# Kernel optimization log

Hardware: AMD Instinct MI355X
Metric: run time of the kernel (lower is better)

Reference implementation:

```python
import jax, jax.numpy as jnp
import numpy as np

B, C, H, W = 8, 16, 512, 512


def setup_inputs() -> dict:
    key = jax.random.key(0)
    k1, k2 = jax.random.split(key)
    src = jax.random.normal(k1, (B, C, H, W), dtype=jnp.float32)
    flow = jax.random.normal(k2, (B, 2, H, W), dtype=jnp.float32)
    return {"src": src, "flow": flow}


def _warp(src, flow):
    b, c, h, w = src.shape
    # identity grid: channel 0 = row index (y), channel 1 = col index (x)
    gy, gx = jnp.meshgrid(jnp.arange(h, dtype=jnp.float32),
                          jnp.arange(w, dtype=jnp.float32), indexing='ij')
    new_y = gy[None, :, :] + flow[:, 0]   # [B,H,W]
    new_x = gx[None, :, :] + flow[:, 1]   # [B,H,W]
    # normalize to [-1,1] (as the torch module does) ...
    ny = 2.0 * (new_y / (h - 1) - 0.5)
    nx = 2.0 * (new_x / (w - 1) - 0.5)
    # ... then un-normalize as grid_sample(align_corners=True) does
    py = (ny + 1.0) * 0.5 * (h - 1)
    px = (nx + 1.0) * 0.5 * (w - 1)
    # padding_mode='border': clip source coords before computing weights
    py = jnp.clip(py, 0.0, h - 1)
    px = jnp.clip(px, 0.0, w - 1)
    y0f = jnp.floor(py)
    x0f = jnp.floor(px)
    wy = (py - y0f)[:, None, :, :]   # [B,1,H,W]
    wx = (px - x0f)[:, None, :, :]
    y0 = jnp.clip(y0f.astype(jnp.int32), 0, h - 1)
    x0 = jnp.clip(x0f.astype(jnp.int32), 0, w - 1)
    y1 = jnp.clip(y0 + 1, 0, h - 1)
    x1 = jnp.clip(x0 + 1, 0, w - 1)

    def gather(s, yi, xi):
        return s[:, yi, xi]  # [C,H,W]

    g = jax.vmap(gather)
    v00 = g(src, y0, x0)
    v01 = g(src, y0, x1)
    v10 = g(src, y1, x0)
    v11 = g(src, y1, x1)
    return (v00 * (1.0 - wy) * (1.0 - wx)
            + v01 * (1.0 - wy) * wx
            + v10 * wy * (1.0 - wx)
            + v11 * wy * wx)


def reference(src, flow):
    return _warp(src, flow)
```

## Files before the change

### kernel.cpp

```cpp
#include <hip/hip_runtime.h>


#define BB 8
#define CC 16
#define HH 512
#define WW 512

typedef float f2u __attribute__((ext_vector_type(2), aligned(4)));

__global__ __launch_bounds__(256) void warp_kernel(
    const float* __restrict__ src,
    const float* __restrict__ flow,
    float* __restrict__ out)
{
    const int HW = HH * WW;
    const int NWG = (BB * HW) / 256;
    const int CHUNK = NWG / 8;

    int bid = (int)blockIdx.x;
    int swz = (bid & 7) * CHUNK + (bid >> 3);

    int b   = swz >> 10;
    int til = swz & 1023;
    int ty  = til >> 5;
    int tx  = til & 31;
    int t   = (int)threadIdx.x;
    int h   = (ty << 4) + (t >> 4);
    int w   = (tx << 4) + (t & 15);
    int hw  = (h << 9) + w;

    const float* fb = flow + (size_t)b * 2 * HW;
    float f0 = __builtin_nontemporal_load(fb + hw);
    float f1 = __builtin_nontemporal_load(fb + HW + hw);

    float py = fminf(fmaxf((float)h + f0, 0.0f), (float)(HH - 1));
    float px = fminf(fmaxf((float)w + f1, 0.0f), (float)(WW - 1));

    int yl = min((int)py, HH - 2);
    int xl = min((int)px, WW - 2);
    float wy = py - (float)yl;
    float wx = px - (float)xl;

    float w00 = (1.0f - wy) * (1.0f - wx);
    float w01 = (1.0f - wy) * wx;
    float w10 = wy * (1.0f - wx);
    float w11 = wy * wx;

    int u0 = (yl << 9) + xl;
    int u1 = u0 + WW;

    const float* sb = src + (size_t)b * CC * HW;
    float*       ob = out + (size_t)b * CC * HW;

    f2u r0[CC], r1[CC];
    #pragma unroll
    for (int c = 0; c < CC; ++c) {
        const float* sc = sb + c * HW;
        r0[c] = *reinterpret_cast<const f2u*>(sc + u0);
        r1[c] = *reinterpret_cast<const f2u*>(sc + u1);
    }
    __builtin_amdgcn_sched_barrier(0);

    #pragma unroll
    for (int c = 0; c < CC; ++c) {
        float v = r0[c].x * w00 + r0[c].y * w01
                + r1[c].x * w10 + r1[c].y * w11;
        __builtin_nontemporal_store(v, ob + c * HW + hw);
    }
}

extern "C" void kernel_launch(void* const* d_in, const int* in_sizes, int n_in,
                              void* d_out, int out_size, void* d_ws, size_t ws_size,
                              hipStream_t stream) {
    const float* src  = (const float*)d_in[0];
    const float* flow = (const float*)d_in[1];
    float* out = (float*)d_out;

    const int n_pix = BB * HH * WW;
    dim3 block(256);
    dim3 grid(n_pix / 256);
    warp_kernel<<<grid, block, 0, stream>>>(src, flow, out);
}
```

Baseline: 287.9 us.

## Stage source window in LDS with double-buffered channel loop for bilinear warp

Each workgroup now covers an 8x32 pixel tile and cooperatively loads a 16x64 source window per channel into shared memory. The window is anchored at the block-wide minimum row index, found with a wave shuffle reduction. Bilinear taps are read from LDS when they fall inside the window and fall back to global loads otherwise. The next channel's window is prefetched into a second buffer while the current one is consumed, which removes the redundant uncoalesced gathers, at the cost of a __syncthreads per channel and loss of the fully unrolled independent load batch.

```diff
diff --git a/kernel.cpp b/kernel.cpp
--- a/kernel.cpp
+++ b/kernel.cpp
@@ -5,28 +5,32 @@
 #define CC 16
 #define HH 512
 #define WW 512
+#define HW (HH*WW)
+
+#define NR   16
+#define NCOL 64
+#define LST  68
 
 typedef float f2u __attribute__((ext_vector_type(2), aligned(4)));
+typedef float f4u __attribute__((ext_vector_type(4), aligned(16)));
 
 __global__ __launch_bounds__(256) void warp_kernel(
     const float* __restrict__ src,
     const float* __restrict__ flow,
     float* __restrict__ out)
 {
-    const int HW = HH * WW;
-    const int NWG = (BB * HW) / 256;
-    const int CHUNK = NWG / 8;
+    __shared__ float tile[2][NR * LST];
+    __shared__ int red[4];
 
     int bid = (int)blockIdx.x;
-    int swz = (bid & 7) * CHUNK + (bid >> 3);
-
+    int swz = (bid & 7) * 1024 + (bid >> 3);
     int b   = swz >> 10;
     int til = swz & 1023;
-    int ty  = til >> 5;
-    int tx  = til & 31;
+    int hb  = (til >> 4) << 3;
+    int wb  = (til & 15) << 5;
     int t   = (int)threadIdx.x;
-    int h   = (ty << 4) + (t >> 4);
-    int w   = (tx << 4) + (t & 15);
+    int h   = hb + (t >> 5);
+    int w   = wb + (t & 31);
     int hw  = (h << 9) + w;
 
     const float* fb = flow + (size_t)b * 2 * HW;
@@ -38,34 +42,55 @@
 
     int yl = min((int)py, HH - 2);
     int xl = min((int)px, WW - 2);
-    float wy = py - (float)yl;
-    float wx = px - (float)xl;
-
+    float wy = py - (float)yl, wx = px - (float)xl;
     float w00 = (1.0f - wy) * (1.0f - wx);
     float w01 = (1.0f - wy) * wx;
     float w10 = wy * (1.0f - wx);
     float w11 = wy * wx;
 
+    int mn = yl;
+    #pragma unroll
+    for (int off = 32; off; off >>= 1) mn = min(mn, __shfl_xor(mn, off));
+    if ((t & 63) == 0) red[t >> 6] = mn;
+    __syncthreads();
+    int ys = min(min(min(red[0], red[1]), min(red[2], red[3])), HH - NR);
+
+    int cs = min(max(wb - 16, 0), WW - NCOL);
+    int loff  = (yl - ys) * LST + (xl - cs);
+    bool valid = ((yl - ys) <= NR - 2) & ((unsigned)(xl - cs) <= NCOL - 2);
     int u0 = (yl << 9) + xl;
-    int u1 = u0 + WW;
 
-    const float* sb = src + (size_t)b * CC * HW;
-    float*       ob = out + (size_t)b * CC * HW;
+    int rr  = t >> 4, ck = (t & 15) << 2;
+    int lso = rr * LST + ck;
+    const float* sst = src + (size_t)b * CC * HW + (size_t)(ys + rr) * WW + cs + ck;
+    const float* sg  = src + (size_t)b * CC * HW;
+    float*       ob  = out + (size_t)b * CC * HW + hw;
 
-    f2u r0[CC], r1[CC];
-    #pragma unroll
+    *reinterpret_cast<f4u*>(&tile[0][lso]) = *reinterpret_cast<const f4u*>(sst);
+    __syncthreads();
+
     for (int c = 0; c < CC; ++c) {
-        const float* sc = sb + c * HW;
-        r0[c] = *reinterpret_cast<const f2u*>(sc + u0);
-        r1[c] = *reinterpret_cast<const f2u*>(sc + u1);
-    }
-    __builtin_amdgcn_sched_barrier(0);
+        f4u nx;
+        if (c + 1 < CC) nx = *reinterpret_cast<const f4u*>(sst + (size_t)(c + 1) * HW);
 
-    #pragma unroll
-    for (int c = 0; c < CC; ++c) {
-        float v = r0[c].x * w00 + r0[c].y * w01
-                + r1[c].x * w10 + r1[c].y * w11;
-        __builtin_nontemporal_store(v, ob + c * HW + hw);
+        const float* tl = tile[c & 1];
+        float v;
+        if (valid) {
+            f2u a = *reinterpret_cast<const f2u*>(&tl[loff]);
+            f2u d = *reinterpret_cast<const f2u*>(&tl[loff + LST]);
+            v = a.x * w00 + a.y * w01 + d.x * w10 + d.y * w11;
+        } else {
+            const float* s = sg + (size_t)c * HW;
+            f2u a = *reinterpret_cast<const f2u*>(s + u0);
+            f2u d = *reinterpret_cast<const f2u*>(s + u0 + WW);
+            v = a.x * w00 + a.y * w01 + d.x * w10 + d.y * w11;
+        }
+        __builtin_nontemporal_store(v, ob + (size_t)c * HW);
+
+        if (c + 1 < CC) {
+            *reinterpret_cast<f4u*>(&tile[(c + 1) & 1][lso]) = nx;
+            __syncthreads();
+        }
     }
 }
 
@@ -76,8 +101,7 @@
     const float* flow = (const float*)d_in[1];
     float* out = (float*)d_out;
 
-    const int n_pix = BB * HH * WW;
     dim3 block(256);
-    dim3 grid(n_pix / 256);
+    dim3 grid(8192);
     warp_kernel<<<grid, block, 0, stream>>>(src, flow, out);
 }
```

Result: faster. 267.6 us (-7.0%).
